# Kernel tuning notes

Hardware: AMD Instinct MI355X
Metric: run time of the kernel (lower is better)

Reference implementation:

```python
import jax, jax.numpy as jnp
import numpy as np

L = 6          # n_layers
V = 512        # vocab_size
D = 768        # n_embd == d_model
P = 768        # proj_size
H = 12         # num_heads
HD = P // H    # head dim = 64
FF = 4 * D     # MLP hidden = 3072
BLOCK = 1024   # block_size
B, T = 8, 1024
LN_EPS = 1e-5


def _layernorm(x, g, b):
    mu = jnp.mean(x, axis=-1, keepdims=True)
    var = jnp.mean(jnp.square(x - mu), axis=-1, keepdims=True)
    return (x - mu) * jax.lax.rsqrt(var + LN_EPS) * g + b


def setup_inputs() -> dict:
    key = jax.random.key(0)
    ks = iter(jax.random.split(key, 32))
    s = 0.02

    def rn(shape):
        return (jax.random.normal(next(ks), shape, jnp.float32) * s)

    inp = {
        "idx": jax.random.randint(next(ks), (B, T), 0, V),
        "attn_mask": jnp.ones((B, T), jnp.float32),
        "tok_emb": rn((V, D)),
        "pos_emb": rn((1, BLOCK, D)),
        # per-layer params stacked on leading L axis
        "ln1_g": jnp.ones((L, D)), "ln1_b": jnp.zeros((L, D)),
        "Wq": rn((L, D, P)), "bq": jnp.zeros((L, P)),
        "Wk": rn((L, D, P)), "bk": jnp.zeros((L, P)),
        "Wv": rn((L, D, P)), "bv": jnp.zeros((L, P)),
        "Wo": rn((L, P, D)), "bo": jnp.zeros((L, D)),
        "ln2_g": jnp.ones((L, D)), "ln2_b": jnp.zeros((L, D)),
        "W1": rn((L, D, FF)), "b1": jnp.zeros((L, FF)),
        "W2": rn((L, FF, D)), "b2": jnp.zeros((L, D)),
        "lnf_g": jnp.ones((D,)), "lnf_b": jnp.zeros((D,)),
        "W_out": rn((D, V)),  # logits head, no bias
    }
    return inp


def reference(idx, attn_mask, tok_emb, pos_emb, ln1_g, ln1_b, Wq, bq, Wk, bk,
              Wv, bv, Wo, bo, ln2_g, ln2_b, W1, b1, W2, b2, lnf_g, lnf_b, W_out):
    Bc, Tc = idx.shape
    x = tok_emb[idx] + pos_emb[:, :Tc]  # [B,T,D]  (dropout: eval mode, identity)

    tril = jnp.tril(jnp.ones((Tc, Tc), jnp.float32))
    # torch.minimum(look_ahead_mask, attn_mask.view(B,1,1,T))
    mask = jnp.minimum(tril[None, None], attn_mask[:, None, None, :])  # [B,1,T,T]
    neg_mask = mask == 0
    scale = 1.0 / np.sqrt(HD)

    layer_params = {
        "ln1_g": ln1_g, "ln1_b": ln1_b, "Wq": Wq, "bq": bq, "Wk": Wk, "bk": bk,
        "Wv": Wv, "bv": bv, "Wo": Wo, "bo": bo, "ln2_g": ln2_g, "ln2_b": ln2_b,
        "W1": W1, "b1": b1, "W2": W2, "b2": b2,
    }

    def block(x, p):
        h = _layernorm(x, p["ln1_g"], p["ln1_b"])
        q = (h @ p["Wq"] + p["bq"]).reshape(Bc, Tc, H, HD)
        k = (h @ p["Wk"] + p["bk"]).reshape(Bc, Tc, H, HD)
        v = (h @ p["Wv"] + p["bv"]).reshape(Bc, Tc, H, HD)
        att = jnp.einsum("bqhd,bkhd->bhqk", q, k) * scale
        att = jnp.where(neg_mask, -jnp.inf, att)
        w = jax.nn.softmax(att, axis=-1)  # attn dropout: identity in eval
        y = jnp.einsum("bhqk,bkhd->bqhd", w, v).reshape(Bc, Tc, P)
        x = x + (y @ p["Wo"] + p["bo"])
        h2 = _layernorm(x, p["ln2_g"], p["ln2_b"])
        m = jax.nn.gelu(h2 @ p["W1"] + p["b1"], approximate=False) @ p["W2"] + p["b2"]
        return x + m

    def step(x, p):
        return block(x, p), None

    x, _ = jax.lax.scan(step, x, layer_params)
    x = _layernorm(x, lnf_g, lnf_b)
    logits = x @ W_out  # [B,T,V]
    return logits
```

## Files before the change

kernel.cpp:

```cpp
#include <hip/hip_runtime.h>
#include <stdint.h>

#define LY 6
#define VOC 512
#define DM 768
#define NH 12
#define HD 64
#define FFD 3072
#define BB 8
#define TT 1024
#define ROWS (BB*TT)

typedef short bf16x8 __attribute__((ext_vector_type(8)));
typedef float f32x4 __attribute__((ext_vector_type(4)));
typedef unsigned short u16x4 __attribute__((ext_vector_type(4)));

#if __has_builtin(__builtin_amdgcn_exp2f)
#define EXP2 __builtin_amdgcn_exp2f
#else
#define EXP2 exp2f
#endif

__device__ __forceinline__ unsigned short f2bf(float f) {
    union { float f; uint32_t u; } v; v.f = f;
    uint32_t r = v.u + 0x7FFFu + ((v.u >> 16) & 1u);
    return (unsigned short)(r >> 16);
}

__device__ __forceinline__ uint32_t f2u(float f) {
    union { float f; uint32_t u; } v; v.f = f;
    return v.u;
}

__device__ __forceinline__ void gl2lds16(const void* g, void* lds) {
    __builtin_amdgcn_global_load_lds(
        (const __attribute__((address_space(1))) uint32_t*)g,
        (__attribute__((address_space(3))) uint32_t*)lds,
        16, 0, 0);
}

__global__ void transpose_w(const float* __restrict__ src, unsigned short* __restrict__ dst,
                            int K, int N, long sls, long dls, int noff) {
    src += (long)blockIdx.z * sls;
    dst += (long)blockIdx.z * dls;
    const int k0 = blockIdx.y * 32, n0 = blockIdx.x * 32;
    __shared__ float tile[32][33];
    const int tx = threadIdx.x, ty = threadIdx.y;
#pragma unroll
    for (int i = 0; i < 4; ++i)
        tile[ty*4+i][tx] = src[(long)(k0 + ty*4 + i) * N + n0 + tx];
    __syncthreads();
#pragma unroll
    for (int i = 0; i < 4; ++i)
        dst[(long)(noff + n0 + ty*4 + i) * K + k0 + tx] = f2bf(tile[tx][ty*4+i]);
}

__global__ void pack_bqkv(const float* __restrict__ bq, const float* __restrict__ bk,
                          const float* __restrict__ bv, float* __restrict__ dst) {
    int i = blockIdx.x * 256 + threadIdx.x;
    if (i >= LY * 2304) return;
    int l = i / 2304, c = i % 2304;
    const float* s = (c < 768) ? bq : (c < 1536 ? bk : bv);
    dst[i] = s[l * 768 + (c % 768)];
}

__global__ __launch_bounds__(256) void embed_kernel(const int* __restrict__ idx,
        const float* __restrict__ tok, const float* __restrict__ pos, float* __restrict__ x) {
    const int g = blockIdx.x * 256 + threadIdx.x;
    const int row = g / 192, c = (g % 192) * 4;
    const int t = row & (TT - 1);
    const int tk = idx[row];
    const f32x4 a = *(const f32x4*)(tok + (long)tk * DM + c);
    const f32x4 p = *(const f32x4*)(pos + (long)t * DM + c);
    f32x4 o = a + p;
    *(f32x4*)(x + (long)row * DM + c) = o;
}

__global__ __launch_bounds__(256) void ln_kernel(const float* __restrict__ x,
        const float* __restrict__ gg, const float* __restrict__ bb,
        unsigned short* __restrict__ out) {
    const int row = (blockIdx.x * 256 + threadIdx.x) >> 6;
    const int lane = threadIdx.x & 63;
    const float* xr = x + (long)row * DM;
    f32x4 v[3];
#pragma unroll
    for (int i = 0; i < 3; ++i) v[i] = *(const f32x4*)(xr + i * 256 + lane * 4);
    float s = 0.f;
#pragma unroll
    for (int i = 0; i < 3; ++i) s += v[i][0] + v[i][1] + v[i][2] + v[i][3];
#pragma unroll
    for (int m = 1; m < 64; m <<= 1) s += __shfl_xor(s, m);
    const float mu = s * (1.f / 768.f);
    float q = 0.f;
#pragma unroll
    for (int i = 0; i < 3; ++i)
#pragma unroll
        for (int j = 0; j < 4; ++j) { float d = v[i][j] - mu; q += d * d; }
#pragma unroll
    for (int m = 1; m < 64; m <<= 1) q += __shfl_xor(q, m);
    const float rs = rsqrtf(q * (1.f / 768.f) + 1e-5f);
#pragma unroll
    for (int i = 0; i < 3; ++i) {
        u16x4 o;
#pragma unroll
        for (int j = 0; j < 4; ++j) {
            const int c = i * 256 + lane * 4 + j;
            o[j] = f2bf((v[i][j] - mu) * rs * gg[c] + bb[c]);
        }
        *(u16x4*)(out + (long)row * DM + i * 256 + lane * 4) = o;
    }
}

template <int EP>
__global__ __launch_bounds__(256)
void gemm128(const unsigned short* __restrict__ A, const unsigned short* __restrict__ Bt,
             const float* __restrict__ bias, const float* __restrict__ res,
             void* __restrict__ Cout, int M, int N, int K,
             unsigned short* __restrict__ aux) {
    __shared__ alignas(16) short As[128 * 64];
    __shared__ alignas(16) short Bs[128 * 64];
    const int tid = threadIdx.x;
    const int w = tid >> 6, lane = tid & 63, quad = lane >> 4, r = lane & 15;
    const int wm = w >> 1, wn = w & 1;
    const long rb = (long)blockIdx.x * 128;
    const long cb = (long)blockIdx.y * 128;

    f32x4 acc[4][4];
    const f32x4 z4 = {0.f, 0.f, 0.f, 0.f};
#pragma unroll
    for (int i = 0; i < 4; ++i)
#pragma unroll
        for (int j = 0; j < 4; ++j) acc[i][j] = z4;

    const int lrow = lane >> 3;
    const int lblk = (lane & 7) ^ lrow;

    for (int k0 = 0; k0 < K; k0 += 64) {
#pragma unroll
        for (int i = 0; i < 4; ++i) {
            const int c = i * 4 + w;
            gl2lds16(A + (rb + 8 * c + lrow) * (long)K + k0 + lblk * 8, (char*)As + c * 1024);
            gl2lds16(Bt + (cb + 8 * c + lrow) * (long)K + k0 + lblk * 8, (char*)Bs + c * 1024);
        }
        __builtin_amdgcn_s_waitcnt(0);
        __syncthreads();
#pragma unroll
        for (int kk = 0; kk < 2; ++kk) {
            bf16x8 af[4], bfr[4];
#pragma unroll
            for (int mi = 0; mi < 4; ++mi) {
                const int row = wm * 64 + mi * 16 + r;
                af[mi] = *(const bf16x8*)((const char*)As + row * 128 + (((kk * 4 + quad) ^ (row & 7)) * 16));
            }
#pragma unroll
            for (int ni = 0; ni < 4; ++ni) {
                const int col = wn * 64 + ni * 16 + r;
                bfr[ni] = *(const bf16x8*)((const char*)Bs + col * 128 + (((kk * 4 + quad) ^ (col & 7)) * 16));
            }
#pragma unroll
            for (int mi = 0; mi < 4; ++mi)
#pragma unroll
                for (int ni = 0; ni < 4; ++ni)
                    acc[mi][ni] = __builtin_amdgcn_mfma_f32_16x16x32_bf16(af[mi], bfr[ni], acc[mi][ni], 0, 0, 0);
        }
        __syncthreads();
    }

    if (EP == 4 && cb >= 1536) {
#pragma unroll
        for (int ni = 0; ni < 4; ++ni) {
            const int col = (int)cb + wn * 64 + ni * 16 + r;
            const float bv = bias[col];
            const int c = col - 1536, hh = c >> 6, dd = c & 63;
#pragma unroll
            for (int mi = 0; mi < 4; ++mi) {
                const int row0 = (int)rb + wm * 64 + mi * 16 + quad * 4;
                const int bb2 = row0 >> 10, t = row0 & 1023;
                u16x4 o;
#pragma unroll
                for (int reg = 0; reg < 4; ++reg) o[reg] = f2bf(acc[mi][ni][reg] + bv);
                *(u16x4*)(aux + (long)((bb2 * NH + hh) * 64 + dd) * TT + t) = o;
            }
        }
        return;
    }

#pragma unroll
    for (int ni = 0; ni < 4; ++ni) {
        const long col = cb + wn * 64 + ni * 16 + r;
        const float bv = (EP == 3) ? 0.f : bias[col];
#pragma unroll
        for (int mi = 0; mi < 4; ++mi) {
            const long row0 = rb + wm * 64 + mi * 16 + quad * 4;
#pragma unroll
            for (int reg = 0; reg < 4; ++reg) {
                const long off = (row0 + reg) * (long)N + col;
                float v = acc[mi][ni][reg] + bv;
                if (EP == 0 || EP == 4) {
                    ((unsigned short*)Cout)[off] = f2bf(v);
                } else if (EP == 1) {
                    v = 0.5f * v * (1.f + erff(v * 0.70710678118654752f));
                    ((unsigned short*)Cout)[off] = f2bf(v);
                } else if (EP == 2) {
                    ((float*)Cout)[off] = res[off] + v;
                } else {
                    ((float*)Cout)[off] = v;
                }
            }
        }
    }
}

#define C1S 0.18033688011112042f

#define LOADK(KT, KF)                                                                     \
    {                                                                                     \
        const unsigned short* kg_ = qkv + (long)(b * TT + (KT) * 32 + r) * 2304           \
                                    + 768 + h * 64 + quad * 8;                            \
        KF[0][0] = *(const bf16x8*)(kg_);                                                 \
        KF[0][1] = *(const bf16x8*)(kg_ + 32);                                            \
        KF[1][0] = *(const bf16x8*)(kg_ + 16 * 2304);                                     \
        KF[1][1] = *(const bf16x8*)(kg_ + 16 * 2304 + 32);                                \
    }

#define PROCESS(KT, KF, KFN)                                                              \
    {                                                                                     \
        const int kt_ = (KT);                                                             \
        const unsigned short* vg_ = vT + (long)(bh * 64 + r) * TT + kt_ * 32 + quad * 8;  \
        bf16x8 vf_[4];                                                                    \
        vf_[0] = *(const bf16x8*)(vg_);                                                   \
        vf_[1] = *(const bf16x8*)(vg_ + 16 * TT);                                         \
        vf_[2] = *(const bf16x8*)(vg_ + 32 * TT);                                         \
        vf_[3] = *(const bf16x8*)(vg_ + 48 * TT);                                         \
        const f32x4 mk0_ = *(const f32x4*)(amask + b * TT + kt_ * 32 + quad * 4);         \
        const f32x4 mk1_ = *(const f32x4*)(amask + b * TT + kt_ * 32 + 16 + quad * 4);    \
        if (kt_ < strip) LOADK(kt_ + 1, KFN);                                             \
        f32x4 st_[2][2];                                                                  \
        _Pragma("unroll")                                                                 \
        for (int qs = 0; qs < 2; ++qs) {                                                  \
            _Pragma("unroll")                                                             \
            for (int nt = 0; nt < 2; ++nt) {                                              \
                st_[qs][nt] = z4;                                                         \
                st_[qs][nt] = __builtin_amdgcn_mfma_f32_16x16x32_bf16(KF[nt][0], qf[qs][0], st_[qs][nt], 0, 0, 0); \
                st_[qs][nt] = __builtin_amdgcn_mfma_f32_16x16x32_bf16(KF[nt][1], qf[qs][1], st_[qs][nt], 0, 0, 0); \
            }                                                                             \
        }                                                                                 \
        f32x4 mb0_, mb1_;                                                                 \
        _Pragma("unroll")                                                                 \
        for (int j = 0; j < 4; ++j) {                                                     \
            mb0_[j] = (mk0_[j] == 0.f) ? NINF : 0.f;                                      \
            mb1_[j] = (mk1_[j] == 0.f) ? NINF : 0.f;                                      \
        }                                                                                 \
        const bool diag_ = (kt_ == strip);                                                \
        _Pragma("unroll")                                                                 \
        for (int qs = 0; qs < 2; ++qs) {                                                  \
            f32x4 t0_, t1_;                                                               \
            _Pragma("unroll")                                                             \
            for (int j = 0; j < 4; ++j) {                                                 \
                t0_[j] = fmaf(st_[qs][0][j], C1S, mb0_[j]);                               \
                t1_[j] = fmaf(st_[qs][1][j], C1S, mb1_[j]);                               \
            }                                                                             \
            if (diag_) {                                                                  \
                const int qg_ = qs * 16 + r;                                              \
                _Pragma("unroll")                                                         \
                for (int j = 0; j < 4; ++j) {                                             \
                    if (quad * 4 + j > qg_)      t0_[j] = NINF;                           \
                    if (16 + quad * 4 + j > qg_) t1_[j] = NINF;                           \
                }                                                                         \
            }                                                                             \
            float mx_ = fmaxf(fmaxf(fmaxf(t0_[0], t0_[1]), fmaxf(t0_[2], t0_[3])),        \
                              fmaxf(fmaxf(t1_[0], t1_[1]), fmaxf(t1_[2], t1_[3])));       \
            mx_ = fmaxf(mx_, __shfl_xor(mx_, 16));                                        \
            mx_ = fmaxf(mx_, __shfl_xor(mx_, 32));                                        \
            const float mnew_ = fmaxf(m_i[qs], mx_);                                      \
            const float alpha_ = EXP2(m_i[qs] - mnew_);                                   \
            m_i[qs] = mnew_;                                                              \
            f32x4 p0_, p1_;                                                               \
            _Pragma("unroll")                                                             \
            for (int j = 0; j < 4; ++j) {                                                 \
                p0_[j] = EXP2(t0_[j] - mnew_);                                            \
                p1_[j] = EXP2(t1_[j] - mnew_);                                            \
            }                                                                             \
            float rs_ = ((p0_[0] + p0_[1]) + (p0_[2] + p0_[3]))                           \
                      + ((p1_[0] + p1_[1]) + (p1_[2] + p1_[3]));                          \
            rs_ += __shfl_xor(rs_, 16);                                                   \
            rs_ += __shfl_xor(rs_, 32);                                                   \
            l_i[qs] = l_i[qs] * alpha_ + rs_;                                             \
            short* Pq_ = Pb + qs * 512;                                                   \
            const uint2 w0_ = { __builtin_amdgcn_perm(f2u(p0_[1]), f2u(p0_[0]), 0x07060302), \
                                __builtin_amdgcn_perm(f2u(p0_[3]), f2u(p0_[2]), 0x07060302) }; \
            const uint2 w1_ = { __builtin_amdgcn_perm(f2u(p1_[1]), f2u(p1_[0]), 0x07060302), \
                                __builtin_amdgcn_perm(f2u(p1_[3]), f2u(p1_[2]), 0x07060302) }; \
            const int half_ = (quad & 1) * 4;                                             \
            *(uint2*)(Pq_ + r * 32 + ((((quad >> 1)) ^ (r & 3)) << 3) + half_) = w0_;     \
            *(uint2*)(Pq_ + r * 32 + (((2 + (quad >> 1)) ^ (r & 3)) << 3) + half_) = w1_; \
            float al_[4];                                                                 \
            _Pragma("unroll")                                                             \
            for (int reg = 0; reg < 4; ++reg)                                             \
                al_[reg] = __shfl(alpha_, (lane & 48) | (quad * 4 + reg));                \
            _Pragma("unroll")                                                             \
            for (int dt = 0; dt < 4; ++dt)                                                \
                _Pragma("unroll")                                                         \
                for (int reg = 0; reg < 4; ++reg) acc[qs][dt][reg] *= al_[reg];           \
            const bf16x8 pf_ = *(const bf16x8*)(Pq_ + r * 32 + ((quad ^ (r & 3)) << 3));  \
            _Pragma("unroll")                                                             \
            for (int dt = 0; dt < 4; ++dt)                                                \
                acc[qs][dt] = __builtin_amdgcn_mfma_f32_16x16x32_bf16(pf_, vf_[dt], acc[qs][dt], 0, 0, 0); \
        }                                                                                 \
    }

__global__ __launch_bounds__(256, 3)
void attn_kernel(const unsigned short* __restrict__ qkv, const unsigned short* __restrict__ vT,
                 const float* __restrict__ amask, unsigned short* __restrict__ y) {
    const int bh = blockIdx.x, b = bh / NH, h = bh % NH;
    const int tid = threadIdx.x, w = tid >> 6, lane = tid & 63, quad = lane >> 4, r = lane & 15;
    const int strip = w * 8 + blockIdx.y;
    const int q0 = strip * 32;

    __shared__ alignas(16) short Pall[4 * 2 * 512];
    short* Pb = Pall + w * 1024;

    const float NINF = -__builtin_inff();
    const f32x4 z4 = {0.f, 0.f, 0.f, 0.f};

    bf16x8 qf[2][2];
#pragma unroll
    for (int qs = 0; qs < 2; ++qs)
#pragma unroll
        for (int ks = 0; ks < 2; ++ks)
            qf[qs][ks] = *(const bf16x8*)(qkv + (long)(b * TT + q0 + qs * 16 + r) * 2304
                                          + h * 64 + ks * 32 + quad * 8);

    f32x4 acc[2][4];
    float m_i[2] = {NINF, NINF}, l_i[2] = {0.f, 0.f};
#pragma unroll
    for (int qs = 0; qs < 2; ++qs)
#pragma unroll
        for (int dt = 0; dt < 4; ++dt) acc[qs][dt] = z4;

    bf16x8 kfA[2][2], kfB[2][2];
    LOADK(0, kfA);
    int kt = 0;
    for (;;) {
        PROCESS(kt, kfA, kfB);
        ++kt; if (kt > strip) break;
        PROCESS(kt, kfB, kfA);
        ++kt; if (kt > strip) break;
    }

#pragma unroll
    for (int qs = 0; qs < 2; ++qs) {
        const float inv0 = 1.0f / l_i[qs];
#pragma unroll
        for (int reg = 0; reg < 4; ++reg) {
            const float inv = __shfl(inv0, (lane & 48) | (quad * 4 + reg));
            const long row = b * TT + q0 + qs * 16 + quad * 4 + reg;
#pragma unroll
            for (int dt = 0; dt < 4; ++dt)
                y[row * DM + h * 64 + dt * 16 + r] = f2bf(acc[qs][dt][reg] * inv);
        }
    }
}

extern "C" void kernel_launch(void* const* d_in, const int* in_sizes, int n_in,
                              void* d_out, int out_size, void* d_ws, size_t ws_size,
                              hipStream_t stream) {
    (void)in_sizes; (void)n_in; (void)out_size; (void)ws_size;
    const int*   idx   = (const int*)d_in[0];
    const float* amask = (const float*)d_in[1];
    const float* tok   = (const float*)d_in[2];
    const float* pos   = (const float*)d_in[3];
    const float* ln1g  = (const float*)d_in[4];
    const float* ln1b  = (const float*)d_in[5];
    const float* Wq    = (const float*)d_in[6];
    const float* bq    = (const float*)d_in[7];
    const float* Wk    = (const float*)d_in[8];
    const float* bk    = (const float*)d_in[9];
    const float* Wv    = (const float*)d_in[10];
    const float* bv    = (const float*)d_in[11];
    const float* Wo    = (const float*)d_in[12];
    const float* bo    = (const float*)d_in[13];
    const float* ln2g  = (const float*)d_in[14];
    const float* ln2b  = (const float*)d_in[15];
    const float* W1    = (const float*)d_in[16];
    const float* b1    = (const float*)d_in[17];
    const float* W2    = (const float*)d_in[18];
    const float* b2    = (const float*)d_in[19];
    const float* lnfg  = (const float*)d_in[20];
    const float* lnfb  = (const float*)d_in[21];
    const float* Wout  = (const float*)d_in[22];

    char* ws = (char*)d_ws;
    float* x            = (float*)ws;          ws += (size_t)ROWS * DM * 4;
    unsigned short* h   = (unsigned short*)ws; ws += (size_t)ROWS * DM * 2;
    unsigned short* qkv = (unsigned short*)ws; ws += (size_t)ROWS * 2304 * 2;
    unsigned short* vT  = (unsigned short*)ws; ws += (size_t)ROWS * DM * 2;
    unsigned short* y   = (unsigned short*)ws; ws += (size_t)ROWS * DM * 2;
    unsigned short* m1  = (unsigned short*)ws; ws += (size_t)ROWS * FFD * 2;
    unsigned short* qkvT= (unsigned short*)ws; ws += (size_t)LY * 2304 * DM * 2;
    unsigned short* WoT = (unsigned short*)ws; ws += (size_t)LY * DM * DM * 2;
    unsigned short* W1T = (unsigned short*)ws; ws += (size_t)LY * FFD * DM * 2;
    unsigned short* W2T = (unsigned short*)ws; ws += (size_t)LY * DM * FFD * 2;
    unsigned short* WouT= (unsigned short*)ws; ws += (size_t)VOC * DM * 2;
    float* bqkv         = (float*)ws;          ws += (size_t)LY * 2304 * 4;

    dim3 blk32(32, 8, 1);
    transpose_w<<<dim3(24, 24, LY), blk32, 0, stream>>>(Wq, qkvT, 768, 768, 768L*768, 2304L*768, 0);
    transpose_w<<<dim3(24, 24, LY), blk32, 0, stream>>>(Wk, qkvT, 768, 768, 768L*768, 2304L*768, 768);
    transpose_w<<<dim3(24, 24, LY), blk32, 0, stream>>>(Wv, qkvT, 768, 768, 768L*768, 2304L*768, 1536);
    transpose_w<<<dim3(24, 24, LY), blk32, 0, stream>>>(Wo, WoT, 768, 768, 768L*768, 768L*768, 0);
    transpose_w<<<dim3(96, 24, LY), blk32, 0, stream>>>(W1, W1T, 768, 3072, 768L*3072, 3072L*768, 0);
    transpose_w<<<dim3(24, 96, LY), blk32, 0, stream>>>(W2, W2T, 3072, 768, 3072L*768, 768L*3072, 0);
    transpose_w<<<dim3(16, 24, 1),  blk32, 0, stream>>>(Wout, WouT, 768, 512, 768L*512, 512L*768, 0);
    pack_bqkv<<<dim3(54), 256, 0, stream>>>(bq, bk, bv, bqkv);
    embed_kernel<<<dim3(6144), 256, 0, stream>>>(idx, tok, pos, x);

    for (int l = 0; l < LY; ++l) {
        ln_kernel<<<2048, 256, 0, stream>>>(x, ln1g + l * DM, ln1b + l * DM, h);
        gemm128<4><<<dim3(64, 18), 256, 0, stream>>>(h, qkvT + (size_t)l * 2304 * DM, bqkv + l * 2304,
                                                     nullptr, qkv, ROWS, 2304, DM, vT);
        attn_kernel<<<dim3(96, 8), 256, 0, stream>>>(qkv, vT, amask, y);
        gemm128<2><<<dim3(64, 6), 256, 0, stream>>>(y, WoT + (size_t)l * DM * DM, bo + l * DM,
                                                    x, x, ROWS, DM, DM, nullptr);
        ln_kernel<<<2048, 256, 0, stream>>>(x, ln2g + l * DM, ln2b + l * DM, h);
        gemm128<1><<<dim3(64, 24), 256, 0, stream>>>(h, W1T + (size_t)l * FFD * DM, b1 + l * FFD,
                                                     nullptr, m1, ROWS, FFD, DM, nullptr);
        gemm128<2><<<dim3(64, 6), 256, 0, stream>>>(m1, W2T + (size_t)l * DM * FFD, b2 + l * DM,
                                                    x, x, ROWS, DM, FFD, nullptr);
    }
    ln_kernel<<<2048, 256, 0, stream>>>(x, lnfg, lnfb, h);
    gemm128<3><<<dim3(64, 4), 256, 0, stream>>>(h, WouT, nullptr, nullptr, d_out, ROWS, VOC, DM, nullptr);
}
```

Before: 1.976 ms.

## Transpose MFMA accumulator layout for vectorized epilogue stores and fast GELU

Swaps the MFMA operand order so each lane's accumulator holds four consecutive output columns of one row. This lets bias loads, residual reads and bf16/fp32 stores in the GEMM epilogue be vectorized instead of scalar and strided. The erf-based GELU is replaced with a tanh approximation built from exp2 and a reciprocal. LayerNorm output packing is also vectorized. The tanh GELU deviates slightly from exact erf, and the V-transpose store path becomes strided scalar writes.

```diff
diff --git a/kernel.cpp b/kernel.cpp
--- a/kernel.cpp
+++ b/kernel.cpp
@@ -21,6 +21,12 @@
 #define EXP2 exp2f
 #endif
 
+#if __has_builtin(__builtin_amdgcn_rcpf)
+#define RCP __builtin_amdgcn_rcpf
+#else
+#define RCP(x) (1.0f/(x))
+#endif
+
 __device__ __forceinline__ unsigned short f2bf(float f) {
     union { float f; uint32_t u; } v; v.f = f;
     uint32_t r = v.u + 0x7FFFu + ((v.u >> 16) & 1u);
@@ -30,6 +36,26 @@
 __device__ __forceinline__ uint32_t f2u(float f) {
     union { float f; uint32_t u; } v; v.f = f;
     return v.u;
+}
+
+__device__ __forceinline__ uint32_t bfround(float f) {
+    union { float f; uint32_t u; } v; v.f = f;
+    return v.u + 0x7FFFu + ((v.u >> 16) & 1u);
+}
+
+__device__ __forceinline__ uint2 packbf4(f32x4 v) {
+    uint32_t r0 = bfround(v[0]), r1 = bfround(v[1]), r2 = bfround(v[2]), r3 = bfround(v[3]);
+    uint2 o;
+    o.x = __builtin_amdgcn_perm(r1, r0, 0x07060302);
+    o.y = __builtin_amdgcn_perm(r3, r2, 0x07060302);
+    return o;
+}
+
+__device__ __forceinline__ float fast_gelu(float x) {
+    const float u = x * (0.79788456f + 0.0356774081f * x * x);
+    const float e = EXP2(u * 2.885390082f);
+    const float t = 1.f - 2.f * RCP(e + 1.f);
+    return 0.5f * x * (1.f + t);
 }
 
 __device__ __forceinline__ void gl2lds16(const void* g, void* lds) {
@@ -101,13 +127,12 @@
     const float rs = rsqrtf(q * (1.f / 768.f) + 1e-5f);
 #pragma unroll
     for (int i = 0; i < 3; ++i) {
-        u16x4 o;
-#pragma unroll
-        for (int j = 0; j < 4; ++j) {
-            const int c = i * 256 + lane * 4 + j;
-            o[j] = f2bf((v[i][j] - mu) * rs * gg[c] + bb[c]);
-        }
-        *(u16x4*)(out + (long)row * DM + i * 256 + lane * 4) = o;
+        const f32x4 g4 = *(const f32x4*)(gg + i * 256 + lane * 4);
+        const f32x4 b4 = *(const f32x4*)(bb + i * 256 + lane * 4);
+        f32x4 o;
+#pragma unroll
+        for (int j = 0; j < 4; ++j) o[j] = (v[i][j] - mu) * rs * g4[j] + b4[j];
+        *(uint2*)(out + (long)row * DM + i * 256 + lane * 4) = packbf4(o);
     }
 }
 
@@ -161,51 +186,51 @@
             for (int mi = 0; mi < 4; ++mi)
 #pragma unroll
                 for (int ni = 0; ni < 4; ++ni)
-                    acc[mi][ni] = __builtin_amdgcn_mfma_f32_16x16x32_bf16(af[mi], bfr[ni], acc[mi][ni], 0, 0, 0);
+                    acc[ni][mi] = __builtin_amdgcn_mfma_f32_16x16x32_bf16(bfr[ni], af[mi], acc[ni][mi], 0, 0, 0);
         }
         __syncthreads();
     }
 
     if (EP == 4 && cb >= 1536) {
 #pragma unroll
-        for (int ni = 0; ni < 4; ++ni) {
-            const int col = (int)cb + wn * 64 + ni * 16 + r;
-            const float bv = bias[col];
-            const int c = col - 1536, hh = c >> 6, dd = c & 63;
-#pragma unroll
-            for (int mi = 0; mi < 4; ++mi) {
-                const int row0 = (int)rb + wm * 64 + mi * 16 + quad * 4;
-                const int bb2 = row0 >> 10, t = row0 & 1023;
-                u16x4 o;
-#pragma unroll
-                for (int reg = 0; reg < 4; ++reg) o[reg] = f2bf(acc[mi][ni][reg] + bv);
-                *(u16x4*)(aux + (long)((bb2 * NH + hh) * 64 + dd) * TT + t) = o;
+        for (int ci = 0; ci < 4; ++ci) {
+            const int colb = (int)cb + wn * 64 + ci * 16 + quad * 4;
+            const f32x4 b4 = *(const f32x4*)(bias + colb);
+            const int c = colb - 1536, hh = c >> 6, dd = c & 63;
+#pragma unroll
+            for (int ri = 0; ri < 4; ++ri) {
+                const int row = (int)rb + wm * 64 + ri * 16 + r;
+                const int bb2 = row >> 10, t = row & 1023;
+                unsigned short* vbase = aux + (long)((bb2 * NH + hh) * 64 + dd) * TT + t;
+#pragma unroll
+                for (int reg = 0; reg < 4; ++reg)
+                    vbase[(long)reg * TT] = f2bf(acc[ci][ri][reg] + b4[reg]);
             }
         }
         return;
     }
 
 #pragma unroll
-    for (int ni = 0; ni < 4; ++ni) {
-        const long col = cb + wn * 64 + ni * 16 + r;
-        const float bv = (EP == 3) ? 0.f : bias[col];
-#pragma unroll
-        for (int mi = 0; mi < 4; ++mi) {
-            const long row0 = rb + wm * 64 + mi * 16 + quad * 4;
-#pragma unroll
-            for (int reg = 0; reg < 4; ++reg) {
-                const long off = (row0 + reg) * (long)N + col;
-                float v = acc[mi][ni][reg] + bv;
-                if (EP == 0 || EP == 4) {
-                    ((unsigned short*)Cout)[off] = f2bf(v);
-                } else if (EP == 1) {
-                    v = 0.5f * v * (1.f + erff(v * 0.70710678118654752f));
-                    ((unsigned short*)Cout)[off] = f2bf(v);
-                } else if (EP == 2) {
-                    ((float*)Cout)[off] = res[off] + v;
-                } else {
-                    ((float*)Cout)[off] = v;
-                }
+    for (int ci = 0; ci < 4; ++ci) {
+        const long colb = cb + wn * 64 + ci * 16 + quad * 4;
+        f32x4 b4 = z4;
+        if (EP != 3) b4 = *(const f32x4*)(bias + colb);
+#pragma unroll
+        for (int ri = 0; ri < 4; ++ri) {
+            const long row = rb + wm * 64 + ri * 16 + r;
+            const long off = row * (long)N + colb;
+            f32x4 v = acc[ci][ri] + b4;
+            if (EP == 0 || EP == 4) {
+                *(uint2*)((unsigned short*)Cout + off) = packbf4(v);
+            } else if (EP == 1) {
+#pragma unroll
+                for (int j = 0; j < 4; ++j) v[j] = fast_gelu(v[j]);
+                *(uint2*)((unsigned short*)Cout + off) = packbf4(v);
+            } else if (EP == 2) {
+                const f32x4 rr = *(const f32x4*)(res + off);
+                *(f32x4*)((float*)Cout + off) = v + rr;
+            } else {
+                *(f32x4*)((float*)Cout + off) = v;
             }
         }
     }
```

Result: faster. 1.910 ms (-3.4%).
